# Performance work log

Measured on AMD Instinct MI355X. Metric: run time of the kernel, lower is better.

## Reference

```python
import jax, jax.numpy as jnp
import numpy as np

LEAKY_SLOPE = 0.2  # nn.LeakyReLU(alpha) with alpha=0.2
NEG_MASK = -9e15   # matches -9000000000000000.0 in the torch source


def _leaky_relu(x):
    return jnp.where(x > 0, x, LEAKY_SLOPE * x)


def setup_inputs() -> dict:
    key = jax.random.key(0)
    kh, ka, k0, k1, k2, k3 = jax.random.split(key, 6)
    B, N, D = 512, 256, 128
    hidden = jax.random.normal(kh, (B, N, D), dtype=jnp.float32)
    adj = jax.random.randint(ka, (B, N, N), 0, 5, dtype=jnp.int32)
    a_0 = jax.random.normal(k0, (D, 1), dtype=jnp.float32) * 0.05
    a_1 = jax.random.normal(k1, (D, 1), dtype=jnp.float32) * 0.05
    a_2 = jax.random.normal(k2, (D, 1), dtype=jnp.float32) * 0.05
    a_3 = jax.random.normal(k3, (D, 1), dtype=jnp.float32) * 0.05
    return {"hidden": hidden, "adj": adj, "a_0": a_0, "a_1": a_1, "a_2": a_2, "a_3": a_3}


def reference(hidden, adj, a_0, a_1, a_2, a_3):
    # hidden: [B, N, D]; adj: [B, N, N] int with relation ids in {0..4}
    # Original builds a_input[b,i,j,:] = hidden[b,i,:] * hidden[b,j,:] then
    # e_r = leakyrelu(a_input @ a_r). Equivalent (same math, no N*N*D blowup):
    # e_r[b,i,j] = leakyrelu( sum_d hidden[b,i,d] * a_r[d] * hidden[b,j,d] ).
    h = hidden

    def rel_scores(a_r):
        hw = h * a_r[:, 0][None, None, :]           # [B, N, D]
        return _leaky_relu(jnp.einsum('bid,bjd->bij', hw, h))  # [B, N, N]

    e_0 = rel_scores(a_0)
    e_1 = rel_scores(a_1)
    e_2 = rel_scores(a_2)
    e_3 = rel_scores(a_3)

    scores = jnp.full_like(e_0, NEG_MASK)
    scores = jnp.where(adj == 1, e_0, scores)
    scores = jnp.where(adj == 2, e_1, scores)
    scores = jnp.where(adj == 3, e_2, scores)
    scores = jnp.where(adj == 4, e_3, scores)

    alpha = jax.nn.softmax(scores, axis=-1)         # [B, N, N]
    return jnp.einsum('bij,bjd->bid', alpha, h)     # [B, N, D]
```

## Files before the change

kernel.cpp:

```cpp
#include <hip/hip_runtime.h>
#include <hip/hip_bf16.h>

typedef _Float16 f16x8 __attribute__((ext_vector_type(8)));
typedef float f32x4  __attribute__((ext_vector_type(4)));
typedef __fp16 fp16x2 __attribute__((ext_vector_type(2)));

#define NB 512
#define NN 256
#define ND 128
#define H_STRIDE 136
#define HT_STRIDE 264
#define SMEM_SHORTS (NN*H_STRIDE + ND*HT_STRIDE + 4*ND)
#define SMEM_BYTES (SMEM_SHORTS * 2)

__device__ __forceinline__ unsigned pack_f16(float a, float b) {
    union { fp16x2 v; unsigned u; } x;
    x.v = __builtin_amdgcn_cvt_pkrtz(a, b);
    return x.u;
}
__device__ __forceinline__ float unp_lo(unsigned u) {
    union { unsigned short s; __fp16 h; } x; x.s = (unsigned short)(u & 0xffffu);
    return (float)x.h;
}
__device__ __forceinline__ float unp_hi(unsigned u) {
    union { unsigned short s; __fp16 h; } x; x.s = (unsigned short)(u >> 16);
    return (float)x.h;
}

__global__ __attribute__((amdgpu_flat_work_group_size(512, 512)))
__attribute__((amdgpu_waves_per_eu(2, 2)))
void gat_fused(const float* __restrict__ hidden, const int* __restrict__ adj,
               const float* __restrict__ a0, const float* __restrict__ a1,
               const float* __restrict__ a2, const float* __restrict__ a3,
               float* __restrict__ out)
{
    extern __shared__ short smem[];
    short* s_h  = smem;
    short* s_ht = s_h + NN * H_STRIDE;
    short* s_a  = s_ht + ND * HT_STRIDE;

    const int b    = blockIdx.x;
    const int tid  = threadIdx.x;
    const int wave = tid >> 6;
    const int lane = tid & 63;
    const int c = lane & 15;
    const int g = lane >> 4;

    int srcl[4];
    #pragma unroll
    for (int r = 0; r < 4; ++r) srcl[r] = c + 16 * (((8 * g + 2 * r) & 15) >> 2);

    const float* hb = hidden + (size_t)b * (NN * ND);
    for (int idx = tid * 4; idx < NN * ND; idx += 512 * 4) {
        const float4 v = *(const float4*)(hb + idx);
        const int j = idx >> 7, d = idx & (ND - 1);
        uint2 pkv;
        pkv.x = pack_f16(v.x, v.y);
        pkv.y = pack_f16(v.z, v.w);
        *(uint2*)&s_h[j * H_STRIDE + d] = pkv;
    }
    {
        const float* ap = (tid < 128) ? a0 : (tid < 256) ? a1 : (tid < 384) ? a2 : a3;
        union { __fp16 h; short s; } cv; cv.h = (__fp16)ap[tid & 127];
        s_a[tid] = cv.s;
    }
    __syncthreads();

    #pragma unroll
    for (int iter = 0; iter < 8; ++iter) {
        const int task = wave + 8 * iter;
        const int d0 = (task & 15) * 8;
        const int j0 = (task >> 4) * 64;
        union { short s[8]; uint4 u; } pkv;
        pkv.u = *(const uint4*)&s_h[(j0 + lane) * H_STRIDE + d0];
        #pragma unroll
        for (int e = 0; e < 8; ++e)
            s_ht[(d0 + e) * HT_STRIDE + j0 + lane] = pkv.s[e];
    }
    __syncthreads();

    const int* adj_b = adj + ((size_t)b << 16);
    float* out_b = out + (size_t)b * (NN * ND);

    for (int n = 0; n < 2; ++n) {
        const int it = wave + 8 * n;
        const int ibase = it * 16;

        unsigned avpk4[8];
        #pragma unroll
        for (int jt2 = 0; jt2 < 8; ++jt2) {
            const int4 aA = *(const int4*)&adj_b[(ibase + c) * NN + (2 * jt2) * 16 + 4 * g];
            const int4 aB = *(const int4*)&adj_b[(ibase + c) * NN + (2 * jt2 + 1) * 16 + 4 * g];
            avpk4[jt2] = (unsigned)aA.x | ((unsigned)aA.y << 4) |
                         ((unsigned)aA.z << 8) | ((unsigned)aA.w << 12) |
                         ((unsigned)aB.x << 16) | ((unsigned)aB.y << 20) |
                         ((unsigned)aB.z << 24) | ((unsigned)aB.w << 28);
        }
        __builtin_amdgcn_sched_barrier(0);

        unsigned scp[16][2];
        float m = -3.0e38f;

        {
            f16x8 qs[2][4];
            #pragma unroll
            for (int s = 0; s < 4; ++s) {
                const f16x8 q = *(const f16x8*)&s_h[(ibase + c) * H_STRIDE + s * 32 + g * 8];
                #pragma unroll
                for (int r = 0; r < 2; ++r) {
                    const f16x8 av = *(const f16x8*)&s_a[r * ND + s * 32 + g * 8];
                    qs[r][s] = q * av;
                }
            }
            #pragma unroll
            for (int jt = 0; jt < 16; ++jt) {
                if ((jt & 1) == 0) __builtin_amdgcn_sched_barrier(0);
                const int jbase = jt * 16;
                f32x4 e0 = {0.f,0.f,0.f,0.f}, e1 = {0.f,0.f,0.f,0.f};
                #pragma unroll
                for (int s = 0; s < 4; ++s) {
                    const f16x8 hj = *(const f16x8*)&s_h[(jbase + c) * H_STRIDE + s * 32 + g * 8];
                    e0 = __builtin_amdgcn_mfma_f32_16x16x32_f16(hj, qs[0][s], e0, 0, 0, 0);
                    e1 = __builtin_amdgcn_mfma_f32_16x16x32_f16(hj, qs[1][s], e1, 0, 0, 0);
                }
                const unsigned apk = avpk4[jt >> 1] >> ((jt & 1) * 16);
                float v[4];
                #pragma unroll
                for (int q = 0; q < 4; ++q) {
                    const int a = (apk >> (4 * q)) & 0xf;
                    v[q] = (a == 1) ? e0[q] : (a == 2) ? e1[q] : -9.0e15f;
                }
                scp[jt][0] = pack_f16(v[0], v[1]);
                scp[jt][1] = pack_f16(v[2], v[3]);
            }
        }

        {
            f16x8 qs[2][4];
            #pragma unroll
            for (int s = 0; s < 4; ++s) {
                const f16x8 q = *(const f16x8*)&s_h[(ibase + c) * H_STRIDE + s * 32 + g * 8];
                #pragma unroll
                for (int r = 0; r < 2; ++r) {
                    const f16x8 av = *(const f16x8*)&s_a[(r + 2) * ND + s * 32 + g * 8];
                    qs[r][s] = q * av;
                }
            }
            #pragma unroll
            for (int jt = 0; jt < 16; ++jt) {
                if ((jt & 1) == 0) __builtin_amdgcn_sched_barrier(0);
                const int jbase = jt * 16;
                f32x4 e2 = {0.f,0.f,0.f,0.f}, e3 = {0.f,0.f,0.f,0.f};
                #pragma unroll
                for (int s = 0; s < 4; ++s) {
                    const f16x8 hj = *(const f16x8*)&s_h[(jbase + c) * H_STRIDE + s * 32 + g * 8];
                    e2 = __builtin_amdgcn_mfma_f32_16x16x32_f16(hj, qs[0][s], e2, 0, 0, 0);
                    e3 = __builtin_amdgcn_mfma_f32_16x16x32_f16(hj, qs[1][s], e3, 0, 0, 0);
                }
                const unsigned apk = avpk4[jt >> 1] >> ((jt & 1) * 16);
                float v[4];
                #pragma unroll
                for (int q = 0; q < 4; ++q) {
                    const int a = (apk >> (4 * q)) & 0xf;
                    const float prev = (q == 0) ? unp_lo(scp[jt][0]) :
                                       (q == 1) ? unp_hi(scp[jt][0]) :
                                       (q == 2) ? unp_lo(scp[jt][1]) : unp_hi(scp[jt][1]);
                    float e = (a == 3) ? e2[q] : (a == 4) ? e3[q] : prev;
                    e = e > 0.f ? e : 0.2f * e;
                    m = fmaxf(m, e);
                    v[q] = e;
                }
                scp[jt][0] = pack_f16(v[0], v[1]);
                scp[jt][1] = pack_f16(v[2], v[3]);
            }
        }

        m = fmaxf(m, __shfl_xor(m, 16));
        m = fmaxf(m, __shfl_xor(m, 32));
        float sum = 0.f;
        #pragma unroll
        for (int jt = 0; jt < 16; ++jt) {
            const float p0 = __expf(unp_lo(scp[jt][0]) - m);
            const float p1 = __expf(unp_hi(scp[jt][0]) - m);
            const float p2 = __expf(unp_lo(scp[jt][1]) - m);
            const float p3 = __expf(unp_hi(scp[jt][1]) - m);
            sum += (p0 + p1) + (p2 + p3);
            scp[jt][0] = pack_f16(p0, p1);
            scp[jt][1] = pack_f16(p2, p3);
        }
        sum += __shfl_xor(sum, 16);
        sum += __shfl_xor(sum, 32);
        const float rinv = 1.f / sum;
        float rq[4];
        #pragma unroll
        for (int q = 0; q < 4; ++q) rq[q] = __shfl(rinv, 4 * g + q, 64);

        f32x4 oacc[8];
        #pragma unroll
        for (int dt = 0; dt < 8; ++dt) oacc[dt] = (f32x4){0.f,0.f,0.f,0.f};
        #pragma unroll
        for (int ph = 0; ph < 8; ++ph) {
            union { unsigned u[4]; f16x8 v; } pa;
            #pragma unroll
            for (int r = 0; r < 4; ++r) {
                const unsigned lo = __shfl(scp[2 * ph][r & 1], srcl[r], 64);
                const unsigned hi = __shfl(scp[2 * ph + 1][r & 1], srcl[r], 64);
                pa.u[r] = (g >= 2) ? hi : lo;
            }
            #pragma unroll
            for (int dt = 0; dt < 8; ++dt) {
                const f16x8 vb = *(const f16x8*)
                    &s_ht[(dt * 16 + c) * HT_STRIDE + ph * 32 + g * 8];
                oacc[dt] = __builtin_amdgcn_mfma_f32_16x16x32_f16(pa.v, vb, oacc[dt], 0, 0, 0);
            }
        }

        #pragma unroll
        for (int dt = 0; dt < 8; ++dt)
            #pragma unroll
            for (int q = 0; q < 4; ++q)
                out_b[(ibase + 4 * g + q) * ND + dt * 16 + c] = oacc[dt][q] * rq[q];
    }
}

extern "C" void kernel_launch(void* const* d_in, const int* in_sizes, int n_in,
                              void* d_out, int out_size, void* d_ws, size_t ws_size,
                              hipStream_t stream) {
    const float* hidden = (const float*)d_in[0];
    const int*   adjp   = (const int*)d_in[1];
    const float* a0 = (const float*)d_in[2];
    const float* a1 = (const float*)d_in[3];
    const float* a2 = (const float*)d_in[4];
    const float* a3 = (const float*)d_in[5];
    float* outp = (float*)d_out;

    (void)hipFuncSetAttribute((const void*)gat_fused,
                              hipFuncAttributeMaxDynamicSharedMemorySize, SMEM_BYTES);
    gat_fused<<<dim3(NB), dim3(512), SMEM_BYTES, stream>>>(hidden, adjp, a0, a1, a2, a3, outp);
}
```

Measured before the change: 82.97 us.

## Use MFMA-native LDS layout with transpose reads, drop the separate transposed copy

```diff
diff --git a/kernel.cpp b/kernel.cpp
--- a/kernel.cpp
+++ b/kernel.cpp
@@ -4,13 +4,13 @@
 typedef _Float16 f16x8 __attribute__((ext_vector_type(8)));
 typedef float f32x4  __attribute__((ext_vector_type(4)));
 typedef __fp16 fp16x2 __attribute__((ext_vector_type(2)));
+typedef unsigned uint32x2 __attribute__((ext_vector_type(2)));
 
 #define NB 512
 #define NN 256
 #define ND 128
-#define H_STRIDE 136
-#define HT_STRIDE 264
-#define SMEM_SHORTS (NN*H_STRIDE + ND*HT_STRIDE + 4*ND)
+#define SH_ELEMS (NN*ND)
+#define SMEM_SHORTS (SH_ELEMS + 4*ND)
 #define SMEM_BYTES (SMEM_SHORTS * 2)
 
 __device__ __forceinline__ unsigned pack_f16(float a, float b) {
@@ -35,9 +35,8 @@
                float* __restrict__ out)
 {
     extern __shared__ short smem[];
-    short* s_h  = smem;
-    short* s_ht = s_h + NN * H_STRIDE;
-    short* s_a  = s_ht + ND * HT_STRIDE;
+    short* s_h = smem;
+    short* s_a = s_h + SH_ELEMS;
 
     const int b    = blockIdx.x;
     const int tid  = threadIdx.x;
@@ -50,14 +49,26 @@
     #pragma unroll
     for (int r = 0; r < 4; ++r) srcl[r] = c + 16 * (((8 * g + 2 * r) & 15) >> 2);
 
+    const int e_lane = ((g >> 1) << 9) + (((c >> 2) & 1) << 8) +
+                       ((c >> 3) << 6) + ((c & 3) << 4) + ((g & 1) << 3);
+
     const float* hb = hidden + (size_t)b * (NN * ND);
-    for (int idx = tid * 4; idx < NN * ND; idx += 512 * 4) {
-        const float4 v = *(const float4*)(hb + idx);
-        const int j = idx >> 7, d = idx & (ND - 1);
+    #pragma unroll
+    for (int it2 = 0; it2 < 16; ++it2) {
+        const int lin = it2 * 2048 + tid * 4;
+        const int cc = lin & 15;
+        const int e4 = (lin >> 4) & 3;
+        const int gj = (lin >> 6) & 3;
+        const int h8 = (lin >> 8) & 1;
+        const int dt = (lin >> 9) & 7;
+        const int ph = lin >> 12;
+        const int j = ph * 32 + gj * 8 + h8 * 4 + e4;
+        const int d = dt * 16 + cc;
+        const float4 v = *(const float4*)(hb + j * ND + d);
         uint2 pkv;
         pkv.x = pack_f16(v.x, v.y);
         pkv.y = pack_f16(v.z, v.w);
-        *(uint2*)&s_h[j * H_STRIDE + d] = pkv;
+        *(uint2*)&s_h[lin] = pkv;
     }
     {
         const float* ap = (tid < 128) ? a0 : (tid < 256) ? a1 : (tid < 384) ? a2 : a3;
@@ -66,25 +77,14 @@
     }
     __syncthreads();
 
-    #pragma unroll
-    for (int iter = 0; iter < 8; ++iter) {
-        const int task = wave + 8 * iter;
-        const int d0 = (task & 15) * 8;
-        const int j0 = (task >> 4) * 64;
-        union { short s[8]; uint4 u; } pkv;
-        pkv.u = *(const uint4*)&s_h[(j0 + lane) * H_STRIDE + d0];
-        #pragma unroll
-        for (int e = 0; e < 8; ++e)
-            s_ht[(d0 + e) * HT_STRIDE + j0 + lane] = pkv.s[e];
-    }
-    __syncthreads();
-
+    const unsigned lds_base = (unsigned)(size_t)(void*)s_h;
     const int* adj_b = adj + ((size_t)b << 16);
     float* out_b = out + (size_t)b * (NN * ND);
 
     for (int n = 0; n < 2; ++n) {
         const int it = wave + 8 * n;
         const int ibase = it * 16;
+        const int qoff = e_lane + (it >> 1) * 4096 + (it & 1) * 128;
 
         unsigned avpk4[8];
         #pragma unroll
@@ -105,7 +105,7 @@
             f16x8 qs[2][4];
             #pragma unroll
             for (int s = 0; s < 4; ++s) {
-                const f16x8 q = *(const f16x8*)&s_h[(ibase + c) * H_STRIDE + s * 32 + g * 8];
+                const f16x8 q = *(const f16x8*)&s_h[qoff + s * 1024];
                 #pragma unroll
                 for (int r = 0; r < 2; ++r) {
                     const f16x8 av = *(const f16x8*)&s_a[r * ND + s * 32 + g * 8];
@@ -115,11 +115,11 @@
             #pragma unroll
             for (int jt = 0; jt < 16; ++jt) {
                 if ((jt & 1) == 0) __builtin_amdgcn_sched_barrier(0);
-                const int jbase = jt * 16;
+                const int joff = e_lane + (jt >> 1) * 4096 + (jt & 1) * 128;
                 f32x4 e0 = {0.f,0.f,0.f,0.f}, e1 = {0.f,0.f,0.f,0.f};
                 #pragma unroll
                 for (int s = 0; s < 4; ++s) {
-                    const f16x8 hj = *(const f16x8*)&s_h[(jbase + c) * H_STRIDE + s * 32 + g * 8];
+                    const f16x8 hj = *(const f16x8*)&s_h[joff + s * 1024];
                     e0 = __builtin_amdgcn_mfma_f32_16x16x32_f16(hj, qs[0][s], e0, 0, 0, 0);
                     e1 = __builtin_amdgcn_mfma_f32_16x16x32_f16(hj, qs[1][s], e1, 0, 0, 0);
                 }
@@ -139,7 +139,7 @@
             f16x8 qs[2][4];
             #pragma unroll
             for (int s = 0; s < 4; ++s) {
-                const f16x8 q = *(const f16x8*)&s_h[(ibase + c) * H_STRIDE + s * 32 + g * 8];
+                const f16x8 q = *(const f16x8*)&s_h[qoff + s * 1024];
                 #pragma unroll
                 for (int r = 0; r < 2; ++r) {
                     const f16x8 av = *(const f16x8*)&s_a[(r + 2) * ND + s * 32 + g * 8];
@@ -149,11 +149,11 @@
             #pragma unroll
             for (int jt = 0; jt < 16; ++jt) {
                 if ((jt & 1) == 0) __builtin_amdgcn_sched_barrier(0);
-                const int jbase = jt * 16;
+                const int joff = e_lane + (jt >> 1) * 4096 + (jt & 1) * 128;
                 f32x4 e2 = {0.f,0.f,0.f,0.f}, e3 = {0.f,0.f,0.f,0.f};
                 #pragma unroll
                 for (int s = 0; s < 4; ++s) {
-                    const f16x8 hj = *(const f16x8*)&s_h[(jbase + c) * H_STRIDE + s * 32 + g * 8];
+                    const f16x8 hj = *(const f16x8*)&s_h[joff + s * 1024];
                     e2 = __builtin_amdgcn_mfma_f32_16x16x32_f16(hj, qs[0][s], e2, 0, 0, 0);
                     e3 = __builtin_amdgcn_mfma_f32_16x16x32_f16(hj, qs[1][s], e3, 0, 0, 0);
                 }
@@ -208,10 +208,26 @@
                 pa.u[r] = (g >= 2) ? hi : lo;
             }
             #pragma unroll
-            for (int dt = 0; dt < 8; ++dt) {
-                const f16x8 vb = *(const f16x8*)
-                    &s_ht[(dt * 16 + c) * HT_STRIDE + ph * 32 + g * 8];
-                oacc[dt] = __builtin_amdgcn_mfma_f32_16x16x32_f16(pa.v, vb, oacc[dt], 0, 0, 0);
+            for (int half = 0; half < 2; ++half) {
+                uint32x2 t0[4], t1[4];
+                #pragma unroll
+                for (int k = 0; k < 4; ++k) {
+                    const int dt = half * 4 + k;
+                    const unsigned a = lds_base + (unsigned)((ph * 8 + dt) * 1024 + lane * 8);
+                    asm volatile("ds_read_b64_tr_b16 %0, %1"
+                                 : "=v"(t0[k]) : "v"(a));
+                    asm volatile("ds_read_b64_tr_b16 %0, %1 offset:512"
+                                 : "=v"(t1[k]) : "v"(a));
+                }
+                asm volatile("s_waitcnt lgkmcnt(0)" ::: "memory");
+                __builtin_amdgcn_sched_barrier(0);
+                #pragma unroll
+                for (int k = 0; k < 4; ++k) {
+                    const int dt = half * 4 + k;
+                    union { uint32x2 p[2]; f16x8 v; } vb;
+                    vb.p[0] = t0[k]; vb.p[1] = t1[k];
+                    oacc[dt] = __builtin_amdgcn_mfma_f32_16x16x32_f16(pa.v, vb.v, oacc[dt], 0, 0, 0);
+                }
             }
         }
 
```

New measurement: 148.9 us. 1.79x slower.
